# Kernel tuning notes

Hardware: AMD Instinct MI355X
Metric: run time of the kernel (lower is better)

The kernel has to match this reference:

```python
import jax, jax.numpy as jnp
import numpy as np

T, D, F, E, K = 8192, 1024, 512, 8, 2


def setup_inputs() -> dict:
    key = jax.random.key(0)
    k0, k1, k2, k3, k4 = jax.random.split(key, 5)
    hidden_states = jax.random.normal(k0, (T, D), dtype=jnp.float32)
    top_k_index = jax.random.randint(k1, (T, K), 0, E)
    top_k_weights = jax.random.uniform(k2, (T, K), dtype=jnp.float32)
    gate_up_proj = jax.random.normal(k3, (E, 2 * F, D), dtype=jnp.float32) * 0.02
    down_proj = jax.random.normal(k4, (E, D, F), dtype=jnp.float32) * 0.02
    return dict(hidden_states=hidden_states, top_k_index=top_k_index,
                top_k_weights=top_k_weights, gate_up_proj=gate_up_proj,
                down_proj=down_proj)


def reference(hidden_states, top_k_index, top_k_weights, gate_up_proj, down_proj):
    # hidden_states: [T, D]; top_k_index/weights: [T, K]
    # gate_up_proj: [E, 2F, D]; down_proj: [E, D, F]
    num_experts = gate_up_proj.shape[0]
    out = jnp.zeros_like(hidden_states)
    for e in range(num_experts):  # fixed small expert set
        # combined routing weight for expert e per token (sums duplicate k-slots,
        # matching index_add_ of per-slot contributions of identical expert output)
        w_e = jnp.sum(jnp.where(top_k_index == e, top_k_weights, 0.0), axis=-1)  # [T]
        gu = hidden_states @ gate_up_proj[e].T          # [T, 2F]
        gate, up = jnp.split(gu, 2, axis=-1)            # [T, F] each
        act = jax.nn.silu(gate) * up                    # SiLU-mul (LigerSiLUMulFunction)
        out = out + (act @ down_proj[e].T) * w_e[:, None]
    return out
```

## Files before the change

### kernel.cpp

```cpp
#include <hip/hip_runtime.h>
#include <cstdint>
#include <cstddef>

#define T_TOK 8192
#define DIM   1024
#define FF    512
#define NE    8
#define NSLOT 16384
#define BM    128
#define MAXBLK (NSLOT / BM + NE)
#define BM1   256
#define MAXB1 (NSLOT / BM1 + NE)

typedef short s16x8 __attribute__((ext_vector_type(8)));
typedef float f32x4 __attribute__((ext_vector_type(4)));

__device__ __forceinline__ unsigned int f2bf(float f) {
    union { float f; unsigned int u; } v; v.f = f;
    return (v.u + 0x7FFFu + ((v.u >> 16) & 1u)) >> 16;
}
__device__ __forceinline__ float bf2f(unsigned short b) {
    union { unsigned int u; float f; } v; v.u = ((unsigned int)b) << 16;
    return v.f;
}
__device__ __forceinline__ int pack2(float a, float b) {
    return (int)f2bf(a) | ((int)f2bf(b) << 16);
}
__device__ __forceinline__ int4 cvt8(const float* p) {
    float4 x = *(const float4*)p;
    float4 y = *(const float4*)(p + 4);
    int4 r;
    r.x = pack2(x.x, x.y); r.y = pack2(x.z, x.w);
    r.z = pack2(y.x, y.y); r.w = pack2(y.z, y.w);
    return r;
}

__device__ __forceinline__ void gload16(const unsigned short* g, unsigned short* l) {
    __builtin_amdgcn_global_load_lds(
        (const __attribute__((address_space(1))) void*)g,
        (__attribute__((address_space(3))) void*)l, 16, 0, 0);
}

__global__ __launch_bounds__(256) void route_count(const int* __restrict__ idx,
                                                   int* __restrict__ partial) {
    __shared__ int cnt[NE];
    const int tid = threadIdx.x;
    if (tid < NE) cnt[tid] = 0;
    __syncthreads();
    atomicAdd(&cnt[idx[blockIdx.x * 256 + tid]], 1);
    __syncthreads();
    if (tid < NE) partial[blockIdx.x * NE + tid] = cnt[tid];
}

__global__ void route_scan(const int* __restrict__ partial, int* offsets, int* cursor,
                           int* blk_e, int* blk_by, int* blk_e1, int* blk_by1) {
    __shared__ int counts_s[NE];
    const int tid = threadIdx.x;
    if (tid < NE) {
        int s = 0;
        for (int b = 0; b < 64; ++b) s += partial[b * NE + tid];
        counts_s[tid] = s;
    }
    __syncthreads();
    if (tid == 0) {
        int acc = 0, nb = 0, nb1 = 0;
        for (int e = 0; e < NE; ++e) {
            offsets[e] = acc; cursor[e] = acc;
            const int nby = (counts_s[e] + BM - 1) / BM;
            for (int b = 0; b < nby; ++b) { blk_e[nb] = e; blk_by[nb] = b; ++nb; }
            const int nby1 = (counts_s[e] + BM1 - 1) / BM1;
            for (int b = 0; b < nby1; ++b) { blk_e1[nb1] = e; blk_by1[nb1] = b; ++nb1; }
            acc += counts_s[e];
        }
        offsets[NE] = acc;
        for (int b = nb; b < MAXBLK; ++b) { blk_e[b] = -1; blk_by[b] = 0; }
        for (int b = nb1; b < MAXB1; ++b) { blk_e1[b] = -1; blk_by1[b] = 0; }
    }
}
__global__ void route_scatter(const int* __restrict__ idx, int* cursor,
                              int* row_slot, int* slot_pos) {
    int s = blockIdx.x * 256 + threadIdx.x;
    if (s < NSLOT) {
        int e = idx[s];
        int p = atomicAdd(&cursor[e], 1);
        row_slot[p] = s;
        slot_pos[s] = p;
    }
}

__global__ void cvt_all(const float* __restrict__ h, const float* __restrict__ g,
                        const float* __restrict__ d,
                        unsigned short* __restrict__ hb, unsigned short* __restrict__ gb,
                        unsigned short* __restrict__ db) {
    const int N1 = T_TOK * DIM / 8;
    const int N2 = NE * 2 * FF * DIM / 8;
    const int N3 = NE * DIM * FF / 8;
    const int stride = gridDim.x * 256;
    for (int i = blockIdx.x * 256 + threadIdx.x; i < N1 + N2 + N3; i += stride) {
        const float* s; unsigned short* o; int j;
        if (i < N1)            { s = h; o = hb; j = i; }
        else if (i < N1 + N2)  { s = g; o = gb; j = i - N1; }
        else                   { s = d; o = db; j = i - N1 - N2; }
        *(int4*)(o + (size_t)j * 8) = cvt8(s + (size_t)j * 8);
    }
}


#define G1_STAGE(BA, BB, T) do {                                                        \
    const int kn_ = (T) * 64;                                                           \
    _Pragma("unroll") for (int i_ = 0; i_ < 4; ++i_)                                    \
        gload16(hb + aoff[i_] + kn_, (BA) + (wv * 64 + i_ * 512) * 8);                  \
    _Pragma("unroll") for (int i_ = 0; i_ < 4; ++i_)                                    \
        gload16(gupb + boff[i_] + kn_, (BB) + (wv * 64 + i_ * 512) * 8);                \
} while (0)

#define G1_COMPUTE(BA, BB) do {                                                         \
    const char* Abc_ = (const char*)(BA);                                               \
    const char* Bbc_ = (const char*)(BB);                                               \
    _Pragma("unroll") for (int kk = 0; kk < 2; ++kk) {                                  \
        const int kc = kk * 4 + (lane >> 4);                                            \
        s16x8 af[8], bg[2], bu[2];                                                      \
        _Pragma("unroll") for (int m = 0; m < 8; ++m) {                                 \
            const int r = wr * 128 + m * 16 + (lane & 15);                              \
            af[m] = *(const s16x8*)(Abc_ + r * 128 + ((kc ^ (r & 7)) << 4)); }          \
        _Pragma("unroll") for (int n = 0; n < 2; ++n) {                                 \
            const int rg = wn * 32 + n * 16 + (lane & 15);                              \
            bg[n] = *(const s16x8*)(Bbc_ + rg * 128 + ((kc ^ (rg & 7)) << 4));          \
            const int ru = rg + 128;                                                    \
            bu[n] = *(const s16x8*)(Bbc_ + ru * 128 + ((kc ^ (ru & 7)) << 4)); }        \
        _Pragma("unroll") for (int m = 0; m < 8; ++m)                                   \
        _Pragma("unroll") for (int n = 0; n < 2; ++n) {                                 \
            ag[m][n] = __builtin_amdgcn_mfma_f32_16x16x32_bf16(af[m], bg[n], ag[m][n], 0, 0, 0); \
            au[m][n] = __builtin_amdgcn_mfma_f32_16x16x32_bf16(af[m], bu[n], au[m][n], 0, 0, 0); } \
    }                                                                                   \
} while (0)

__global__ __launch_bounds__(512, 2) void gemm1_256(
    const unsigned short* __restrict__ hb,
    const unsigned short* __restrict__ gupb,
    const int* __restrict__ row_slot,
    const int* __restrict__ offsets,
    const int* __restrict__ blk_e1,
    const int* __restrict__ blk_by1,
    unsigned short* __restrict__ act)
{
    const int e = blk_e1[blockIdx.y];
    if (e < 0) return;
    const int bx      = blockIdx.x;
    const int rowbase = offsets[e] + blk_by1[blockIdx.y] * BM1;
    const int rowlim  = offsets[e + 1] - 1;
    const int nrows   = min(BM1, offsets[e + 1] - rowbase);

    __shared__ __align__(16) unsigned short Ab0[BM1 * 64], Ab1[BM1 * 64];
    __shared__ __align__(16) unsigned short Bb0[256 * 64], Bb1[256 * 64];

    const int tid  = threadIdx.x;
    const int lane = tid & 63;
    const int wv   = tid >> 6;
    const int wr   = wv >> 2;
    const int wn   = wv & 3;

    int aoff[4], boff[4];
#pragma unroll
    for (int i = 0; i < 4; ++i) {
        const int ch = tid + i * 512;
        const int r = ch >> 3, c = ch & 7;
        int grow = rowbase + r; if (grow > rowlim) grow = rowlim;
        const int tok = row_slot[grow] >> 1;
        aoff[i] = tok * DIM + ((c ^ (r & 7)) << 3);
        const int gr = (r < 128) ? (bx * 128 + r) : (FF + bx * 128 + r - 128);
        boff[i] = e * (2 * FF * DIM) + gr * DIM + ((c ^ (r & 7)) << 3);
    }

    const f32x4 zf = {0.f, 0.f, 0.f, 0.f};
    f32x4 ag[8][2], au[8][2];
#pragma unroll
    for (int m = 0; m < 8; ++m)
#pragma unroll
        for (int n = 0; n < 2; ++n) { ag[m][n] = zf; au[m][n] = zf; }

    G1_STAGE(Ab0, Bb0, 0);
    __syncthreads();

#pragma unroll 1
    for (int t = 0; t < DIM / 64; t += 2) {
        G1_STAGE(Ab1, Bb1, t + 1);
        G1_COMPUTE(Ab0, Bb0);
        __syncthreads();
        if (t + 2 < DIM / 64) G1_STAGE(Ab0, Bb0, t + 2);
        G1_COMPUTE(Ab1, Bb1);
        __syncthreads();
    }

#pragma unroll
    for (int m = 0; m < 8; ++m)
#pragma unroll
        for (int n = 0; n < 2; ++n) {
            const int col = bx * 128 + wn * 32 + n * 16 + (lane & 15);
#pragma unroll
            for (int i = 0; i < 4; ++i) {
                const int rl = wr * 128 + m * 16 + ((lane >> 4) << 2) + i;
                if (rl < nrows) {
                    const float g = ag[m][n][i];
                    const float u = au[m][n][i];
                    const float a = (g / (1.f + __expf(-g))) * u;
                    act[(size_t)(rowbase + rl) * FF + col] = (unsigned short)f2bf(a);
                }
            }
        }
}


#define G2_STAGE(BA, BB, T) do {                                                        \
    const int kn_ = (T) * 64;                                                           \
    _Pragma("unroll") for (int i_ = 0; i_ < 4; ++i_)                                    \
        gload16(act + aoff[i_] + kn_, (BA) + (wv * 64 + i_ * 256) * 8);                 \
    _Pragma("unroll") for (int i_ = 0; i_ < 4; ++i_)                                    \
        gload16(downb + boff[i_] + kn_, (BB) + (wv * 64 + i_ * 256) * 8);               \
} while (0)

#define G2_COMPUTE(BA, BB) do {                                                         \
    const char* Abc_ = (const char*)(BA);                                               \
    const char* Bbc_ = (const char*)(BB);                                               \
    _Pragma("unroll") for (int kk = 0; kk < 2; ++kk) {                                  \
        const int kc = kk * 4 + (lane >> 4);                                            \
        s16x8 af[4], bf[4];                                                             \
        _Pragma("unroll") for (int m = 0; m < 4; ++m) {                                 \
            const int r = wr * 64 + m * 16 + (lane & 15);                               \
            af[m] = *(const s16x8*)(Abc_ + r * 128 + ((kc ^ (r & 7)) << 4)); }          \
        _Pragma("unroll") for (int n = 0; n < 4; ++n) {                                 \
            const int r = wc * 64 + n * 16 + (lane & 15);                               \
            bf[n] = *(const s16x8*)(Bbc_ + r * 128 + ((kc ^ (r & 7)) << 4)); }          \
        _Pragma("unroll") for (int m = 0; m < 4; ++m)                                   \
        _Pragma("unroll") for (int n = 0; n < 4; ++n)                                   \
            acc[m][n] = __builtin_amdgcn_mfma_f32_16x16x32_bf16(af[m], bf[n], acc[m][n], 0, 0, 0); \
    }                                                                                   \
} while (0)

template <int MODE>
__global__ __launch_bounds__(256) void gemm2_slot(
    const unsigned short* __restrict__ act,
    const unsigned short* __restrict__ downb,
    const int* __restrict__ row_slot,
    const int* __restrict__ offsets,
    const int* __restrict__ blk_e,
    const int* __restrict__ blk_by,
    void* __restrict__ outslot)
{
    const int e = blk_e[blockIdx.y];
    if (e < 0) return;
    const int bx      = blockIdx.x;
    const int lby     = blk_by[blockIdx.y];
    const int rowbase = offsets[e] + lby * BM;
    const int nrows   = min(BM, offsets[e + 1] - rowbase);
    const int rowlim  = offsets[e + 1] - 1;

    __shared__ __align__(16) unsigned short Ab0[BM * 64], Ab1[BM * 64];
    __shared__ __align__(16) unsigned short Bb0[128 * 64], Bb1[128 * 64];

    const int tid  = threadIdx.x;
    const int lane = tid & 63;
    const int wv   = tid >> 6;
    const int wr   = wv >> 1, wc = wv & 1;

    int aoff[4];
#pragma unroll
    for (int i = 0; i < 4; ++i) {
        const int ch = tid + i * 256;
        const int r = ch >> 3, c = ch & 7;
        int grow = rowbase + r; if (grow > rowlim) grow = rowlim;
        aoff[i] = grow * FF + ((c ^ (r & 7)) << 3);
    }
    int boff[4];
#pragma unroll
    for (int i = 0; i < 4; ++i) {
        const int ch = tid + i * 256;
        const int r = ch >> 3, c = ch & 7;
        boff[i] = e * (DIM * FF) + (bx * 128 + r) * FF + ((c ^ (r & 7)) << 3);
    }

    const f32x4 zf = {0.f, 0.f, 0.f, 0.f};
    f32x4 acc[4][4];
#pragma unroll
    for (int m = 0; m < 4; ++m)
#pragma unroll
        for (int n = 0; n < 4; ++n) acc[m][n] = zf;

    G2_STAGE(Ab0, Bb0, 0);
    __syncthreads();

#pragma unroll 1
    for (int t = 0; t < FF / 64; t += 2) {
        G2_STAGE(Ab1, Bb1, t + 1);
        G2_COMPUTE(Ab0, Bb0);
        __syncthreads();
        if (t + 2 < FF / 64) G2_STAGE(Ab0, Bb0, t + 2);
        G2_COMPUTE(Ab1, Bb1);
        __syncthreads();
    }

#pragma unroll
    for (int m = 0; m < 4; ++m)
#pragma unroll
        for (int i = 0; i < 4; ++i) {
            const int rl = wr * 64 + m * 16 + ((lane >> 4) << 2) + i;
            if (rl < nrows) {
                const size_t base = (size_t)(rowbase + rl) * DIM + bx * 128 + wc * 64 + (lane & 15);
                if (MODE == 1) {
                    float* o = (float*)outslot + base;
#pragma unroll
                    for (int n = 0; n < 4; ++n) o[n * 16] = acc[m][n][i];
                } else {
                    unsigned short* o = (unsigned short*)outslot + base;
#pragma unroll
                    for (int n = 0; n < 4; ++n) o[n * 16] = (unsigned short)f2bf(acc[m][n][i]);
                }
            }
        }
}

template <int MODE>
__global__ __launch_bounds__(256) void combine_k(
    const void* __restrict__ outslot,
    const int* __restrict__ slot_pos,
    const float* __restrict__ tkw,
    float* __restrict__ out)
{
    const int i = blockIdx.x * 256 + threadIdx.x;
    const int t = i >> 7;
    const int d = (i & 127) << 3;
    const int p0 = slot_pos[2 * t], p1 = slot_pos[2 * t + 1];
    const float w0 = tkw[2 * t],    w1 = tkw[2 * t + 1];
    float r0[8], r1[8];
    if (MODE == 1) {
        const float* s0 = (const float*)outslot + (size_t)p0 * DIM + d;
        const float* s1 = (const float*)outslot + (size_t)p1 * DIM + d;
        float4 a0 = *(const float4*)s0, a1 = *(const float4*)(s0 + 4);
        float4 b0 = *(const float4*)s1, b1 = *(const float4*)(s1 + 4);
        r0[0]=a0.x; r0[1]=a0.y; r0[2]=a0.z; r0[3]=a0.w; r0[4]=a1.x; r0[5]=a1.y; r0[6]=a1.z; r0[7]=a1.w;
        r1[0]=b0.x; r1[1]=b0.y; r1[2]=b0.z; r1[3]=b0.w; r1[4]=b1.x; r1[5]=b1.y; r1[6]=b1.z; r1[7]=b1.w;
    } else {
        const s16x8 a = *(const s16x8*)((const unsigned short*)outslot + (size_t)p0 * DIM + d);
        const s16x8 b = *(const s16x8*)((const unsigned short*)outslot + (size_t)p1 * DIM + d);
#pragma unroll
        for (int j = 0; j < 8; ++j) { r0[j] = bf2f((unsigned short)a[j]); r1[j] = bf2f((unsigned short)b[j]); }
    }
    float4 o0, o1;
    o0.x = w0*r0[0]+w1*r1[0]; o0.y = w0*r0[1]+w1*r1[1]; o0.z = w0*r0[2]+w1*r1[2]; o0.w = w0*r0[3]+w1*r1[3];
    o1.x = w0*r0[4]+w1*r1[4]; o1.y = w0*r0[5]+w1*r1[5]; o1.z = w0*r0[6]+w1*r1[6]; o1.w = w0*r0[7]+w1*r1[7];
    float* op = out + (size_t)t * DIM + d;
    *(float4*)op = o0;
    *(float4*)(op + 4) = o1;
}


__global__ __launch_bounds__(256) void moe_gemm1(
    const float* __restrict__ hidden, const float* __restrict__ gup,
    const int* __restrict__ row_slot, const int* __restrict__ offsets,
    unsigned short* __restrict__ act)
{
    const int e = blockIdx.z;
    const int row0 = offsets[e];
    const int n_e = offsets[e + 1] - row0;
    const int by = blockIdx.y;
    if (by * 128 >= n_e) return;
    const int bx = blockIdx.x;
    __shared__ __align__(16) unsigned short Abuf[128 * 64];
    __shared__ __align__(16) unsigned short Bbuf[128 * 64];
    char* Ab = (char*)Abuf; char* Bb = (char*)Bbuf;
    const int tid = threadIdx.x, lane = tid & 63, wv = tid >> 6;
    const int wr = wv >> 1, wc = wv & 1;
    const float* aptr[4]; const float* bptr[4]; int soff[4];
#pragma unroll
    for (int i = 0; i < 4; ++i) {
        const int chunk = tid + i * 256;
        const int r = chunk >> 3, c = chunk & 7;
        soff[i] = r * 128 + ((c ^ (r & 7)) << 4);
        int rr = by * 128 + r; if (rr >= n_e) rr = n_e - 1;
        const int slot = row_slot[row0 + rr];
        aptr[i] = hidden + (size_t)(slot >> 1) * DIM + c * 8;
        const int gr = (r < 64) ? (bx * 64 + r) : (FF + bx * 64 + (r - 64));
        bptr[i] = gup + (size_t)e * (2 * FF * DIM) + (size_t)gr * DIM + c * 8;
    }
    const f32x4 zf = {0.f, 0.f, 0.f, 0.f};
    f32x4 acc_g[4][2], acc_u[4][2];
#pragma unroll
    for (int m = 0; m < 4; ++m)
#pragma unroll
        for (int n = 0; n < 2; ++n) { acc_g[m][n] = zf; acc_u[m][n] = zf; }
    for (int k0 = 0; k0 < DIM; k0 += 64) {
        __syncthreads();
#pragma unroll
        for (int i = 0; i < 4; ++i) *(int4*)(Ab + soff[i]) = cvt8(aptr[i] + k0);
#pragma unroll
        for (int i = 0; i < 4; ++i) *(int4*)(Bb + soff[i]) = cvt8(bptr[i] + k0);
        __syncthreads();
#pragma unroll
        for (int kk = 0; kk < 2; ++kk) {
            const int kc = kk * 4 + (lane >> 4);
            s16x8 af[4], bg[2], bu[2];
#pragma unroll
            for (int m = 0; m < 4; ++m) {
                const int r = wr * 64 + m * 16 + (lane & 15);
                af[m] = *(const s16x8*)(Ab + r * 128 + ((kc ^ (r & 7)) << 4));
            }
#pragma unroll
            for (int n = 0; n < 2; ++n) {
                const int rg = wc * 32 + n * 16 + (lane & 15);
                bg[n] = *(const s16x8*)(Bb + rg * 128 + ((kc ^ (rg & 7)) << 4));
                const int ru = rg + 64;
                bu[n] = *(const s16x8*)(Bb + ru * 128 + ((kc ^ (ru & 7)) << 4));
            }
#pragma unroll
            for (int m = 0; m < 4; ++m)
#pragma unroll
                for (int n = 0; n < 2; ++n) {
                    acc_g[m][n] = __builtin_amdgcn_mfma_f32_16x16x32_bf16(af[m], bg[n], acc_g[m][n], 0, 0, 0);
                    acc_u[m][n] = __builtin_amdgcn_mfma_f32_16x16x32_bf16(af[m], bu[n], acc_u[m][n], 0, 0, 0);
                }
        }
    }
#pragma unroll
    for (int m = 0; m < 4; ++m)
#pragma unroll
        for (int n = 0; n < 2; ++n) {
            const int col = bx * 64 + wc * 32 + n * 16 + (lane & 15);
#pragma unroll
            for (int i = 0; i < 4; ++i) {
                const int rl = wr * 64 + m * 16 + ((lane >> 4) << 2) + i;
                const int rr = by * 128 + rl;
                if (rr < n_e) {
                    const float g = acc_g[m][n][i];
                    const float u = acc_u[m][n][i];
                    const float a = (g / (1.f + __expf(-g))) * u;
                    act[(size_t)(row0 + rr) * FF + col] = (unsigned short)f2bf(a);
                }
            }
        }
}

__global__ __launch_bounds__(256) void moe_gemm2(
    const unsigned short* __restrict__ act, const float* __restrict__ down,
    const int* __restrict__ row_slot, const int* __restrict__ offsets,
    const float* __restrict__ tkw, float* __restrict__ out)
{
    const int e = blockIdx.z;
    const int row0 = offsets[e];
    const int n_e = offsets[e + 1] - row0;
    const int by = blockIdx.y;
    if (by * 128 >= n_e) return;
    const int bx = blockIdx.x;
    __shared__ __align__(16) unsigned short Abuf[128 * 64];
    __shared__ __align__(16) unsigned short Bbuf[128 * 64];
    char* Ab = (char*)Abuf; char* Bb = (char*)Bbuf;
    const int tid = threadIdx.x, lane = tid & 63, wv = tid >> 6;
    const int wr = wv >> 1, wc = wv & 1;
    const unsigned short* aptr[4]; const float* bptr[4]; int soff[4];
#pragma unroll
    for (int i = 0; i < 4; ++i) {
        const int chunk = tid + i * 256;
        const int r = chunk >> 3, c = chunk & 7;
        soff[i] = r * 128 + ((c ^ (r & 7)) << 4);
        int rr = by * 128 + r; if (rr >= n_e) rr = n_e - 1;
        aptr[i] = act + (size_t)(row0 + rr) * FF + c * 8;
        bptr[i] = down + (size_t)e * (DIM * FF) + (size_t)(bx * 128 + r) * FF + c * 8;
    }
    const f32x4 zf = {0.f, 0.f, 0.f, 0.f};
    f32x4 acc[4][4];
#pragma unroll
    for (int m = 0; m < 4; ++m)
#pragma unroll
        for (int n = 0; n < 4; ++n) acc[m][n] = zf;
    for (int k0 = 0; k0 < FF; k0 += 64) {
        __syncthreads();
#pragma unroll
        for (int i = 0; i < 4; ++i) *(int4*)(Ab + soff[i]) = *(const int4*)(aptr[i] + k0);
#pragma unroll
        for (int i = 0; i < 4; ++i) *(int4*)(Bb + soff[i]) = cvt8(bptr[i] + k0);
        __syncthreads();
#pragma unroll
        for (int kk = 0; kk < 2; ++kk) {
            const int kc = kk * 4 + (lane >> 4);
            s16x8 af[4], bf[4];
#pragma unroll
            for (int m = 0; m < 4; ++m) {
                const int r = wr * 64 + m * 16 + (lane & 15);
                af[m] = *(const s16x8*)(Ab + r * 128 + ((kc ^ (r & 7)) << 4));
            }
#pragma unroll
            for (int n = 0; n < 4; ++n) {
                const int r = wc * 64 + n * 16 + (lane & 15);
                bf[n] = *(const s16x8*)(Bb + r * 128 + ((kc ^ (r & 7)) << 4));
            }
#pragma unroll
            for (int m = 0; m < 4; ++m)
#pragma unroll
                for (int n = 0; n < 4; ++n)
                    acc[m][n] = __builtin_amdgcn_mfma_f32_16x16x32_bf16(af[m], bf[n], acc[m][n], 0, 0, 0);
        }
    }
#pragma unroll
    for (int m = 0; m < 4; ++m)
#pragma unroll
        for (int i = 0; i < 4; ++i) {
            const int rl = wr * 64 + m * 16 + ((lane >> 4) << 2) + i;
            const int rr = by * 128 + rl;
            if (rr < n_e) {
                const int slot = row_slot[row0 + rr];
                const float w = tkw[slot];
                float* orow = out + (size_t)(slot >> 1) * DIM + bx * 128 + wc * 64 + (lane & 15);
#pragma unroll
                for (int n = 0; n < 4; ++n)
                    unsafeAtomicAdd(orow + n * 16, acc[m][n][i] * w);
            }
        }
}

extern "C" void kernel_launch(void* const* d_in, const int* in_sizes, int n_in,
                              void* d_out, int out_size, void* d_ws, size_t ws_size,
                              hipStream_t stream)
{
    const float* hidden = (const float*)d_in[0];
    const int*   idx    = (const int*)  d_in[1];
    const float* tkw    = (const float*)d_in[2];
    const float* gup    = (const float*)d_in[3];
    const float* down   = (const float*)d_in[4];
    float* out = (float*)d_out;

    const size_t ACT = (size_t)NSLOT * FF * 2;
    const size_t HB  = (size_t)T_TOK * DIM * 2;
    const size_t GB  = (size_t)NE * 2 * FF * DIM * 2;
    const size_t DB  = (size_t)NE * DIM * FF * 2;
    const size_t RS  = (size_t)NSLOT * 4;
    const size_t SP  = (size_t)NSLOT * 4;
    const size_t CTRL = 8192;
    const size_t OS32 = (size_t)NSLOT * DIM * 4;
    const size_t OS16 = (size_t)NSLOT * DIM * 2;
    char* ws = (char*)d_ws;
    unsigned short* act = (unsigned short*)ws;

    const size_t base_need = ACT + HB + GB + DB + RS + SP + CTRL;
    int mode;
    if      (ws_size >= base_need + OS32) mode = 1;
    else if (ws_size >= base_need + OS16) mode = 2;
    else if (ws_size >= ACT + RS + SP + CTRL) mode = 0;
    else mode = -1;
    if (mode < 0) return;

    unsigned short *hb = nullptr, *gb = nullptr, *db = nullptr;
    int *row_slot, *ctrl; void* outslot = nullptr;
    if (mode == 1 || mode == 2) {
        hb = (unsigned short*)(ws + ACT);
        gb = (unsigned short*)(ws + ACT + HB);
        db = (unsigned short*)(ws + ACT + HB + GB);
        row_slot = (int*)(ws + ACT + HB + GB + DB);
        ctrl     = (int*)(ws + ACT + HB + GB + DB + RS + SP);
        outslot  = (void*)(ws + base_need);
    } else {
        row_slot = (int*)(ws + ACT);
        ctrl     = (int*)(ws + ACT + RS + SP);
    }
    int* slot_pos = row_slot + NSLOT;
    int* offsets = ctrl;
    int* blk_e   = ctrl + 16;
    int* blk_by  = ctrl + 16 + MAXBLK;
    int* blk_e1  = ctrl + 16 + 2 * MAXBLK;
    int* blk_by1 = ctrl + 16 + 2 * MAXBLK + MAXB1;
    int* cursor  = ctrl + 16 + 2 * MAXBLK + 2 * MAXB1;
    int* partial = cursor + 8;

    if (mode == 0)
        hipMemsetAsync(out, 0, (size_t)T_TOK * DIM * sizeof(float), stream);

    route_count  <<<NSLOT / 256, 256, 0, stream>>>(idx, partial);
    route_scan   <<<1, 64, 0, stream>>>(partial, offsets, cursor, blk_e, blk_by, blk_e1, blk_by1);
    route_scatter<<<NSLOT / 256, 256, 0, stream>>>(idx, cursor, row_slot, slot_pos);

    if (mode == 1 || mode == 2) {
        cvt_all<<<2048, 256, 0, stream>>>(hidden, gup, down, hb, gb, db);
        gemm1_256<<<dim3(FF / 128, MAXB1), 512, 0, stream>>>(
            hb, gb, row_slot, offsets, blk_e1, blk_by1, act);
        if (mode == 1) {
            gemm2_slot<1><<<dim3(DIM / 128, MAXBLK), 256, 0, stream>>>(
                act, db, row_slot, offsets, blk_e, blk_by, outslot);
            combine_k<1><<<T_TOK * DIM / 8 / 256, 256, 0, stream>>>(outslot, slot_pos, tkw, out);
        } else {
            gemm2_slot<2><<<dim3(DIM / 128, MAXBLK), 256, 0, stream>>>(
                act, db, row_slot, offsets, blk_e, blk_by, outslot);
            combine_k<2><<<T_TOK * DIM / 8 / 256, 256, 0, stream>>>(outslot, slot_pos, tkw, out);
        }
    } else {
        moe_gemm1<<<dim3(FF / 64, 128, NE), 256, 0, stream>>>(hidden, gup, row_slot, offsets, act);
        moe_gemm2<<<dim3(DIM / 128, 128, NE), 256, 0, stream>>>(act, down, row_slot, offsets, tkw, out);
    }
}
```

Baseline: 213.8 us.

## Prefetch two K-stages ahead with explicit vmcnt waits in both MoE GEMMs

```diff
diff --git a/kernel.cpp b/kernel.cpp
--- a/kernel.cpp
+++ b/kernel.cpp
@@ -14,6 +14,11 @@
 
 typedef short s16x8 __attribute__((ext_vector_type(8)));
 typedef float f32x4 __attribute__((ext_vector_type(4)));
+
+#define VMCNT8() asm volatile("s_waitcnt vmcnt(8)" ::: "memory")
+#define VMCNT0() asm volatile("s_waitcnt vmcnt(0)" ::: "memory")
+#define SBAR()   __builtin_amdgcn_s_barrier()
+#define SFENCE() __builtin_amdgcn_sched_barrier(0)
 
 __device__ __forceinline__ unsigned int f2bf(float f) {
     union { float f; unsigned int u; } v; v.f = f;
@@ -135,6 +140,8 @@
     }                                                                                   \
 } while (0)
 
+#define NT1 (DIM / 64)
+
 __global__ __launch_bounds__(512, 2) void gemm1_256(
     const unsigned short* __restrict__ hb,
     const unsigned short* __restrict__ gupb,
@@ -180,16 +187,21 @@
         for (int n = 0; n < 2; ++n) { ag[m][n] = zf; au[m][n] = zf; }
 
     G1_STAGE(Ab0, Bb0, 0);
-    __syncthreads();
+    G1_STAGE(Ab1, Bb1, 1);
+    VMCNT8(); SBAR(); SFENCE();
 
 #pragma unroll 1
-    for (int t = 0; t < DIM / 64; t += 2) {
-        G1_STAGE(Ab1, Bb1, t + 1);
+    for (int t = 0; t < NT1; t += 2) {
         G1_COMPUTE(Ab0, Bb0);
-        __syncthreads();
-        if (t + 2 < DIM / 64) G1_STAGE(Ab0, Bb0, t + 2);
+        SBAR();
+        if (t + 2 < NT1) { G1_STAGE(Ab0, Bb0, t + 2); VMCNT8(); }
+        else             { VMCNT0(); }
+        SBAR(); SFENCE();
         G1_COMPUTE(Ab1, Bb1);
-        __syncthreads();
+        SBAR();
+        if (t + 3 < NT1) { G1_STAGE(Ab1, Bb1, t + 3); VMCNT8(); }
+        else             { VMCNT0(); }
+        SBAR(); SFENCE();
     }
 
 #pragma unroll
@@ -237,6 +249,8 @@
     }                                                                                   \
 } while (0)
 
+#define NT2 (FF / 64)
+
 template <int MODE>
 __global__ __launch_bounds__(256) void gemm2_slot(
     const unsigned short* __restrict__ act,
@@ -287,16 +301,21 @@
         for (int n = 0; n < 4; ++n) acc[m][n] = zf;
 
     G2_STAGE(Ab0, Bb0, 0);
-    __syncthreads();
+    G2_STAGE(Ab1, Bb1, 1);
+    VMCNT8(); SBAR(); SFENCE();
 
 #pragma unroll 1
-    for (int t = 0; t < FF / 64; t += 2) {
-        G2_STAGE(Ab1, Bb1, t + 1);
+    for (int t = 0; t < NT2; t += 2) {
         G2_COMPUTE(Ab0, Bb0);
-        __syncthreads();
-        if (t + 2 < FF / 64) G2_STAGE(Ab0, Bb0, t + 2);
+        SBAR();
+        if (t + 2 < NT2) { G2_STAGE(Ab0, Bb0, t + 2); VMCNT8(); }
+        else             { VMCNT0(); }
+        SBAR(); SFENCE();
         G2_COMPUTE(Ab1, Bb1);
-        __syncthreads();
+        SBAR();
+        if (t + 3 < NT2) { G2_STAGE(Ab1, Bb1, t + 3); VMCNT8(); }
+        else             { VMCNT0(); }
+        SBAR(); SFENCE();
     }
 
 #pragma unroll
```

Measured after the change: 225.2 us. +5.3%, slower.
